# Performance work log

Hardware: AMD Instinct MI355X
Metric: run time of the kernel (lower is better)

## Reference

```python
import jax, jax.numpy as jnp
import numpy as np

D_IN = 1024
D_OUT = 1024
NUM_HEADS = 16
HEAD_DIM = D_OUT // NUM_HEADS


def setup_inputs() -> dict:
    key = jax.random.key(0)
    k_x, k_q, k_k, k_v, k_o = jax.random.split(key, 5)
    # Xavier-uniform-ish init for weights (stored as [d_in, d_out] for x @ W)
    lim = float(np.sqrt(6.0 / (D_IN + D_OUT)) / np.sqrt(2.0))
    lim_o = float(np.sqrt(6.0 / (D_OUT + D_OUT)))
    return {
        "x": jax.random.normal(k_x, (2, 2048, D_IN), dtype=jnp.float32),
        "W_query": jax.random.uniform(k_q, (D_IN, D_OUT), jnp.float32, -lim, lim),
        "W_key": jax.random.uniform(k_k, (D_IN, D_OUT), jnp.float32, -lim, lim),
        "W_value": jax.random.uniform(k_v, (D_IN, D_OUT), jnp.float32, -lim, lim),
        "W_out": jax.random.uniform(k_o, (D_OUT, D_OUT), jnp.float32, -lim_o, lim_o),
        "b_out": jnp.zeros((D_OUT,), dtype=jnp.float32),
    }


def reference(x, W_query, W_key, W_value, W_out, b_out):
    B, S, _ = x.shape
    scale = 1.0 / np.sqrt(HEAD_DIM)

    def split_heads(t):  # [B,S,D] -> [B,H,S,hd]
        return t.reshape(B, S, NUM_HEADS, HEAD_DIM).transpose(0, 2, 1, 3)

    q = split_heads(x @ W_query)
    k = split_heads(x @ W_key)
    v = split_heads(x @ W_value)

    scores = jnp.einsum("bhqd,bhkd->bhqk", q, k) * scale  # [B,H,S,S]
    causal = jnp.tril(jnp.ones((S, S), dtype=bool))  # True = keep
    scores = jnp.where(causal, scores, -jnp.inf)
    weights = jax.nn.softmax(scores, axis=-1)
    ctx = jnp.einsum("bhqk,bhkd->bhqd", weights, v)
    ctx = ctx.transpose(0, 2, 1, 3).reshape(B, S, D_OUT)
    return ctx @ W_out + b_out
```

## Files before the change

kernel.cpp:

```cpp
#include <hip/hip_runtime.h>
#include <hip/hip_bf16.h>


typedef __bf16 bf16_t;
typedef __bf16 bf16x4 __attribute__((ext_vector_type(4)));
typedef __bf16 bf16x8 __attribute__((ext_vector_type(8)));
typedef float f32x4 __attribute__((ext_vector_type(4)));

__device__ __forceinline__ void barrier_lgkm() {
    asm volatile("s_waitcnt lgkmcnt(0)\n\ts_barrier" ::: "memory");
}

__device__ __forceinline__ float exp_pwrite(f32x4 sc[4], bf16_t* Ps,
                                            int wave, int quad, int l16) {
    float part = 0.f;
    int rowbase = (wave * 16 + l16) * 64;
    int gran = (quad & 1) * 4;
    int chi = quad >> 1;
#pragma unroll
    for (int nt = 0; nt < 4; nt++) {
        f32x4 p;
#pragma unroll
        for (int rr = 0; rr < 4; rr++) {
            p[rr] = __builtin_amdgcn_exp2f(sc[nt][rr]);
            part += p[rr];
        }
        bf16x4 pb;
#pragma unroll
        for (int rr = 0; rr < 4; rr++) pb[rr] = (bf16_t)p[rr];
        int cc = (nt * 2 + chi) ^ (l16 & 7);
        *(bf16x4*)(Ps + rowbase + cc * 8 + gran) = pb;
    }
    part += __shfl_xor(part, 16);
    part += __shfl_xor(part, 32);
    return part;
}

__global__ __launch_bounds__(256) void prep_k(
    const float* __restrict__ x, const float* __restrict__ W0,
    const float* __restrict__ W1, const float* __restrict__ W2,
    const float* __restrict__ W3, bf16_t* __restrict__ xb,
    bf16_t* __restrict__ WTs) {
    __shared__ bf16_t T[64][65];
    int t = threadIdx.x;
    int blk = blockIdx.x;
    if (blk < 4096) {
        int i = blk * 256 + t;
        float4 v = ((const float4*)x)[i];
        bf16x4 o;
        o[0] = (bf16_t)v.x; o[1] = (bf16_t)v.y;
        o[2] = (bf16_t)v.z; o[3] = (bf16_t)v.w;
        ((bf16x4*)xb)[i] = o;
        return;
    }
    int jj = blk - 4096;
    int k0 = (jj & 15) * 64, n0 = ((jj >> 4) & 15) * 64, z = jj >> 8;
    const float* W = (z == 0) ? W0 : (z == 1) ? W1 : (z == 2) ? W2 : W3;
    bf16_t* WT = WTs + (size_t)z * 1048576;
#pragma unroll
    for (int c = 0; c < 4; c++) {
        int idx = c * 256 + t;
        int row = idx >> 4, col4 = (idx & 15) * 4;
        float4 v = *(const float4*)(W + (k0 + row) * 1024 + n0 + col4);
        T[row][col4 + 0] = (bf16_t)v.x;
        T[row][col4 + 1] = (bf16_t)v.y;
        T[row][col4 + 2] = (bf16_t)v.z;
        T[row][col4 + 3] = (bf16_t)v.w;
    }
    __syncthreads();
#pragma unroll
    for (int c = 0; c < 4; c++) {
        int idx = c * 256 + t;
        int nrow = idx >> 4, kc4 = (idx & 15) * 4;
        bf16x4 o;
        o[0] = T[kc4 + 0][nrow];
        o[1] = T[kc4 + 1][nrow];
        o[2] = T[kc4 + 2][nrow];
        o[3] = T[kc4 + 3][nrow];
        *(bf16x4*)(WT + (n0 + nrow) * 1024 + k0 + kc4) = o;
    }
}

__global__ __launch_bounds__(256) void qkv_k(
    const bf16_t* __restrict__ xb, const bf16_t* __restrict__ WTs,
    bf16_t* __restrict__ Qb, bf16_t* __restrict__ Kb, bf16_t* __restrict__ Vb) {
    const int KD = 1024;
    __shared__ __align__(16) bf16_t As[2][4096];
    __shared__ __align__(16) bf16_t Bs[2][4096];
    int tid = threadIdx.x;
    int wave = tid >> 6, lane = tid & 63;
    int quad = lane >> 4, l16 = lane & 15;
    int wm = wave >> 1, wn = wave & 1;
    int z = blockIdx.z;
    const bf16_t* BT = WTs + (size_t)z * 1048576;
    int m0 = blockIdx.x * 128;
    int n0 = blockIdx.y * 128;

    int r = tid >> 2;
    int c8 = (((tid & 3) ^ ((tid >> 3) & 3))) * 8;
    const bf16_t* gA0 = xb + (size_t)(m0 + r) * KD + c8;
    const bf16_t* gA1 = xb + (size_t)(m0 + 64 + r) * KD + c8;
    const bf16_t* gB0 = BT + (size_t)(n0 + r) * KD + c8;
    const bf16_t* gB1 = BT + (size_t)(n0 + 64 + r) * KD + c8;

    f32x4 acc[4][4];
#pragma unroll
    for (int i = 0; i < 4; i++)
#pragma unroll
        for (int j = 0; j < 4; j++) acc[i][j] = (f32x4){0.f, 0.f, 0.f, 0.f};

    int4 sa0 = *(const int4*)gA0, sa1 = *(const int4*)gA1;
    int4 sb0 = *(const int4*)gB0, sb1 = *(const int4*)gB1;
    *(int4*)(As[0] + tid * 8) = sa0;
    *(int4*)(As[0] + 2048 + tid * 8) = sa1;
    *(int4*)(Bs[0] + tid * 8) = sb0;
    *(int4*)(Bs[0] + 2048 + tid * 8) = sb1;
    sa0 = *(const int4*)(gA0 + 32); sa1 = *(const int4*)(gA1 + 32);
    sb0 = *(const int4*)(gB0 + 32); sb1 = *(const int4*)(gB1 + 32);

    int csw = (quad ^ ((l16 >> 1) & 3)) * 8;
#pragma unroll 1
    for (int kk = 0; kk < 32; kk += 2) {
        barrier_lgkm();
        bf16x8 af[4], bfr[4];
#pragma unroll
        for (int mt = 0; mt < 4; mt++)
            af[mt] = *(const bf16x8*)(As[0] + (wm * 64 + mt * 16 + l16) * 32 + csw);
#pragma unroll
        for (int nt = 0; nt < 4; nt++)
            bfr[nt] = *(const bf16x8*)(Bs[0] + (wn * 64 + nt * 16 + l16) * 32 + csw);
        *(int4*)(As[1] + tid * 8) = sa0;
        *(int4*)(As[1] + 2048 + tid * 8) = sa1;
        *(int4*)(Bs[1] + tid * 8) = sb0;
        *(int4*)(Bs[1] + 2048 + tid * 8) = sb1;
        if (kk + 2 < 32) {
            int k0 = (kk + 2) * 32;
            sa0 = *(const int4*)(gA0 + k0); sa1 = *(const int4*)(gA1 + k0);
            sb0 = *(const int4*)(gB0 + k0); sb1 = *(const int4*)(gB1 + k0);
        }
        if (z == 2) {
#pragma unroll
            for (int mt = 0; mt < 4; mt++)
#pragma unroll
                for (int nt = 0; nt < 4; nt++)
                    acc[mt][nt] = __builtin_amdgcn_mfma_f32_16x16x32_bf16(
                        bfr[nt], af[mt], acc[mt][nt], 0, 0, 0);
        } else {
#pragma unroll
            for (int mt = 0; mt < 4; mt++)
#pragma unroll
                for (int nt = 0; nt < 4; nt++)
                    acc[mt][nt] = __builtin_amdgcn_mfma_f32_16x16x32_bf16(
                        af[mt], bfr[nt], acc[mt][nt], 0, 0, 0);
        }
        barrier_lgkm();
#pragma unroll
        for (int mt = 0; mt < 4; mt++)
            af[mt] = *(const bf16x8*)(As[1] + (wm * 64 + mt * 16 + l16) * 32 + csw);
#pragma unroll
        for (int nt = 0; nt < 4; nt++)
            bfr[nt] = *(const bf16x8*)(Bs[1] + (wn * 64 + nt * 16 + l16) * 32 + csw);
        if (kk + 2 < 32) {
            *(int4*)(As[0] + tid * 8) = sa0;
            *(int4*)(As[0] + 2048 + tid * 8) = sa1;
            *(int4*)(Bs[0] + tid * 8) = sb0;
            *(int4*)(Bs[0] + 2048 + tid * 8) = sb1;
            if (kk + 3 < 32) {
                int k0 = (kk + 3) * 32;
                sa0 = *(const int4*)(gA0 + k0); sa1 = *(const int4*)(gA1 + k0);
                sb0 = *(const int4*)(gB0 + k0); sb1 = *(const int4*)(gB1 + k0);
            }
        }
        if (z == 2) {
#pragma unroll
            for (int mt = 0; mt < 4; mt++)
#pragma unroll
                for (int nt = 0; nt < 4; nt++)
                    acc[mt][nt] = __builtin_amdgcn_mfma_f32_16x16x32_bf16(
                        bfr[nt], af[mt], acc[mt][nt], 0, 0, 0);
        } else {
#pragma unroll
            for (int mt = 0; mt < 4; mt++)
#pragma unroll
                for (int nt = 0; nt < 4; nt++)
                    acc[mt][nt] = __builtin_amdgcn_mfma_f32_16x16x32_bf16(
                        af[mt], bfr[nt], acc[mt][nt], 0, 0, 0);
        }
    }

    if (z == 0) {
#pragma unroll
        for (int mt = 0; mt < 4; mt++) {
            int mg_base = m0 + wm * 64 + mt * 16 + quad * 4;
#pragma unroll
            for (int nt = 0; nt < 4; nt++) {
                int ng = n0 + wn * 64 + nt * 16 + l16;
                int h = ng >> 6, d = ng & 63;
#pragma unroll
                for (int rr = 0; rr < 4; rr++) {
                    int mg = mg_base + rr;
                    int b = mg >> 11, s = mg & 2047;
                    Qb[(((size_t)(b * 16 + h) * 2048) + s) * 64 + d] =
                        (bf16_t)acc[mt][nt][rr];
                }
            }
        }
    } else if (z == 1) {
#pragma unroll
        for (int mt = 0; mt < 4; mt++) {
            int mg_base = m0 + wm * 64 + mt * 16 + quad * 4;
#pragma unroll
            for (int nt = 0; nt < 4; nt++) {
                int ng = n0 + wn * 64 + nt * 16 + l16;
                int h = ng >> 6, dd = ng & 63;
#pragma unroll
                for (int rr = 0; rr < 4; rr++) {
                    int mg = mg_base + rr;
                    int b = mg >> 11, sl = mg & 2047;
                    int kt = sl >> 6, row = sl & 63;
                    int cc = (dd >> 3) ^ (row & 7);
                    Kb[(size_t)(b * 16 + h) * 131072 + kt * 4096 + row * 64 +
                       cc * 8 + (dd & 7)] = (bf16_t)acc[mt][nt][rr];
                }
            }
        }
    } else {
#pragma unroll
        for (int mt = 0; mt < 4; mt++) {
            int sg = m0 + wm * 64 + mt * 16 + l16;
            int b = sg >> 11, sl = sg & 2047;
            int kt = sl >> 6, srow = sl & 63;
#pragma unroll
            for (int nt = 0; nt < 4; nt++) {
                int dg_base = n0 + wn * 64 + nt * 16 + quad * 4;
#pragma unroll
                for (int rr = 0; rr < 4; rr++) {
                    int dg = dg_base + rr;
                    int h = dg >> 6, dd = dg & 63;
                    int cc = (srow >> 3) ^ (dd & 7);
                    Vb[(size_t)(b * 16 + h) * 131072 + kt * 4096 + dd * 64 +
                       cc * 8 + (srow & 7)] = (bf16_t)acc[mt][nt][rr];
                }
            }
        }
    }
}

__global__ __launch_bounds__(256) void attn_k(
    const bf16_t* __restrict__ Qb, const bf16_t* __restrict__ Kb,
    const bf16_t* __restrict__ Vb, bf16_t* __restrict__ ctxb) {
    const int S = 2048;
    __shared__ __align__(16) bf16_t Ks[2][4096];
    __shared__ __align__(16) bf16_t Vs[2][4096];
    __shared__ __align__(16) bf16_t Ps[2][4096];
    int tid = threadIdx.x, wave = tid >> 6, lane = tid & 63;
    int quad = lane >> 4, l16 = lane & 15;

    int f = blockIdx.x + 32 * blockIdx.y;
    int g = f >> 8, s = f & 255;
    int qtj = g ? (15 - (s & 15)) : (s & 15);
    int bh = (s >> 4) + 16 * g;
    int h = bh & 15, b = bh >> 4;
    int q0 = qtj * 128;

    const bf16_t* Qbh = Qb + (size_t)bh * S * 64;
    const bf16_t* Kbh = Kb + (size_t)bh * 131072;
    const bf16_t* Vbh = Vb + (size_t)bh * 131072;

    const float qs = 0.125f * 1.44269504f;
    bf16x8 aQ[2][2];
#pragma unroll
    for (int sub = 0; sub < 2; sub++) {
        const bf16_t* rq = Qbh + (size_t)(q0 + sub * 64 + wave * 16 + l16) * 64;
#pragma unroll
        for (int ks = 0; ks < 2; ks++) {
            bf16x8 t = *(const bf16x8*)(rq + ks * 32 + quad * 8);
#pragma unroll
            for (int j = 0; j < 8; j++) t[j] = (bf16_t)((float)t[j] * qs);
            aQ[sub][ks] = t;
        }
    }

    float L[2] = {0.f, 0.f};
    f32x4 O[2][4];
#pragma unroll
    for (int sub = 0; sub < 2; sub++)
#pragma unroll
        for (int i = 0; i < 4; i++) O[sub][i] = (f32x4){0.f, 0.f, 0.f, 0.f};

    int tmax = 2 * qtj + 2;
    int4 ska = *(const int4*)(Kbh + tid * 8);
    int4 skb = *(const int4*)(Kbh + 2048 + tid * 8);
    int4 sva = *(const int4*)(Vbh + tid * 8);
    int4 svb = *(const int4*)(Vbh + 2048 + tid * 8);
    *(int4*)(Ks[0] + tid * 8) = ska; *(int4*)(Ks[0] + 2048 + tid * 8) = skb;
    *(int4*)(Vs[0] + tid * 8) = sva; *(int4*)(Vs[0] + 2048 + tid * 8) = svb;
    ska = *(const int4*)(Kbh + 4096 + tid * 8);
    skb = *(const int4*)(Kbh + 6144 + tid * 8);
    sva = *(const int4*)(Vbh + 4096 + tid * 8);
    svb = *(const int4*)(Vbh + 6144 + tid * 8);

#pragma unroll 1
    for (int kt = 0; kt < tmax; kt++) {
        int cur = kt & 1;
        barrier_lgkm();
        bf16x8 kf[4][2], vf[4][2];
#pragma unroll
        for (int nt = 0; nt < 4; nt++) {
            const bf16_t* krow = Ks[cur] + (nt * 16 + l16) * 64;
            const bf16_t* vrow = Vs[cur] + (nt * 16 + l16) * 64;
#pragma unroll
            for (int ks = 0; ks < 2; ks++) {
                int csw = ((ks * 4 + quad) ^ (l16 & 7)) * 8;
                kf[nt][ks] = *(const bf16x8*)(krow + csw);
                vf[nt][ks] = *(const bf16x8*)(vrow + csw);
            }
        }
        if (kt + 1 < tmax) {
            *(int4*)(Ks[cur ^ 1] + tid * 8) = ska;
            *(int4*)(Ks[cur ^ 1] + 2048 + tid * 8) = skb;
            *(int4*)(Vs[cur ^ 1] + tid * 8) = sva;
            *(int4*)(Vs[cur ^ 1] + 2048 + tid * 8) = svb;
        }
        if (kt + 2 < tmax) {
            const bf16_t* kg = Kbh + (kt + 2) * 4096;
            const bf16_t* vg = Vbh + (kt + 2) * 4096;
            ska = *(const int4*)(kg + tid * 8);
            skb = *(const int4*)(kg + 2048 + tid * 8);
            sva = *(const int4*)(vg + tid * 8);
            svb = *(const int4*)(vg + 2048 + tid * 8);
        }

        bool do_lo = (kt < tmax - 1);
        if (do_lo) {
            f32x4 sc[4];
#pragma unroll
            for (int nt = 0; nt < 4; nt++) {
                f32x4 ss = (f32x4){0.f, 0.f, 0.f, 0.f};
                ss = __builtin_amdgcn_mfma_f32_16x16x32_bf16(kf[nt][0], aQ[0][0], ss, 0, 0, 0);
                ss = __builtin_amdgcn_mfma_f32_16x16x32_bf16(kf[nt][1], aQ[0][1], ss, 0, 0, 0);
                sc[nt] = ss;
            }
            if (kt == tmax - 2) {
                int qg = q0 + wave * 16 + l16;
#pragma unroll
                for (int nt = 0; nt < 4; nt++)
#pragma unroll
                    for (int rr = 0; rr < 4; rr++)
                        if (kt * 64 + nt * 16 + quad * 4 + rr > qg) sc[nt][rr] = -1e30f;
            }
            L[0] += exp_pwrite(sc, Ps[0], wave, quad, l16);
        }
        {
            f32x4 sc[4];
#pragma unroll
            for (int nt = 0; nt < 4; nt++) {
                f32x4 ss = (f32x4){0.f, 0.f, 0.f, 0.f};
                ss = __builtin_amdgcn_mfma_f32_16x16x32_bf16(kf[nt][0], aQ[1][0], ss, 0, 0, 0);
                ss = __builtin_amdgcn_mfma_f32_16x16x32_bf16(kf[nt][1], aQ[1][1], ss, 0, 0, 0);
                sc[nt] = ss;
            }
            if (kt == tmax - 1) {
                int qg = q0 + 64 + wave * 16 + l16;
#pragma unroll
                for (int nt = 0; nt < 4; nt++)
#pragma unroll
                    for (int rr = 0; rr < 4; rr++)
                        if (kt * 64 + nt * 16 + quad * 4 + rr > qg) sc[nt][rr] = -1e30f;
            }
            L[1] += exp_pwrite(sc, Ps[1], wave, quad, l16);
        }

#pragma unroll
        for (int ks = 0; ks < 2; ks++) {
            int csw = ((ks * 4 + quad) ^ (l16 & 7)) * 8;
            bf16x8 aPhi = *(const bf16x8*)(Ps[1] + (wave * 16 + l16) * 64 + csw);
            bf16x8 aPlo;
            if (do_lo) aPlo = *(const bf16x8*)(Ps[0] + (wave * 16 + l16) * 64 + csw);
#pragma unroll
            for (int nt = 0; nt < 4; nt++) {
                O[1][nt] = __builtin_amdgcn_mfma_f32_16x16x32_bf16(aPhi, vf[nt][ks],
                                                                   O[1][nt], 0, 0, 0);
                if (do_lo)
                    O[0][nt] = __builtin_amdgcn_mfma_f32_16x16x32_bf16(aPlo, vf[nt][ks],
                                                                       O[0][nt], 0, 0, 0);
            }
        }
    }

#pragma unroll
    for (int sub = 0; sub < 2; sub++) {
        float il[4];
#pragma unroll
        for (int rr = 0; rr < 4; rr++) il[rr] = 1.f / __shfl(L[sub], quad * 4 + rr);
#pragma unroll
        for (int nt = 0; nt < 4; nt++) {
#pragma unroll
            for (int rr = 0; rr < 4; rr++) {
                int qoff = q0 + sub * 64 + wave * 16 + quad * 4 + rr;
                int col = h * 64 + nt * 16 + l16;
                ctxb[(size_t)(b * 2048 + qoff) * 1024 + col] =
                    (bf16_t)(O[sub][nt][rr] * il[rr]);
            }
        }
    }
}

__global__ __launch_bounds__(256) void out_k(
    const bf16_t* __restrict__ ctxb, const bf16_t* __restrict__ WoT,
    const float* __restrict__ bo, float* __restrict__ out) {
    const int KD = 1024;
    __shared__ __align__(16) bf16_t As[2][2048];
    __shared__ __align__(16) bf16_t Bs[2][4096];
    int tid = threadIdx.x;
    int wave = tid >> 6, lane = tid & 63;
    int quad = lane >> 4, l16 = lane & 15;
    int wm = wave >> 1, wn = wave & 1;
    int m0 = blockIdx.x * 64;
    int n0 = blockIdx.y * 128;

    int r = tid >> 2;
    int c8 = (((tid & 3) ^ ((tid >> 3) & 3))) * 8;
    const bf16_t* gA  = ctxb + (size_t)(m0 + r) * KD + c8;
    const bf16_t* gB0 = WoT + (size_t)(n0 + r) * KD + c8;
    const bf16_t* gB1 = WoT + (size_t)(n0 + 64 + r) * KD + c8;

    f32x4 acc[2][4];
#pragma unroll
    for (int i = 0; i < 2; i++)
#pragma unroll
        for (int j = 0; j < 4; j++) acc[i][j] = (f32x4){0.f, 0.f, 0.f, 0.f};

    int4 sa = *(const int4*)gA;
    int4 sb0 = *(const int4*)gB0, sb1 = *(const int4*)gB1;
    *(int4*)(As[0] + tid * 8) = sa;
    *(int4*)(Bs[0] + tid * 8) = sb0;
    *(int4*)(Bs[0] + 2048 + tid * 8) = sb1;
    sa = *(const int4*)(gA + 32);
    sb0 = *(const int4*)(gB0 + 32); sb1 = *(const int4*)(gB1 + 32);

    int csw = (quad ^ ((l16 >> 1) & 3)) * 8;
#pragma unroll 1
    for (int kk = 0; kk < 32; kk += 2) {
        barrier_lgkm();
        bf16x8 af[2], bfr[4];
#pragma unroll
        for (int mt = 0; mt < 2; mt++)
            af[mt] = *(const bf16x8*)(As[0] + (wm * 32 + mt * 16 + l16) * 32 + csw);
#pragma unroll
        for (int nt = 0; nt < 4; nt++)
            bfr[nt] = *(const bf16x8*)(Bs[0] + (wn * 64 + nt * 16 + l16) * 32 + csw);
        *(int4*)(As[1] + tid * 8) = sa;
        *(int4*)(Bs[1] + tid * 8) = sb0;
        *(int4*)(Bs[1] + 2048 + tid * 8) = sb1;
        if (kk + 2 < 32) {
            int k0 = (kk + 2) * 32;
            sa = *(const int4*)(gA + k0);
            sb0 = *(const int4*)(gB0 + k0); sb1 = *(const int4*)(gB1 + k0);
        }
#pragma unroll
        for (int mt = 0; mt < 2; mt++)
#pragma unroll
            for (int nt = 0; nt < 4; nt++)
                acc[mt][nt] = __builtin_amdgcn_mfma_f32_16x16x32_bf16(
                    af[mt], bfr[nt], acc[mt][nt], 0, 0, 0);
        barrier_lgkm();
#pragma unroll
        for (int mt = 0; mt < 2; mt++)
            af[mt] = *(const bf16x8*)(As[1] + (wm * 32 + mt * 16 + l16) * 32 + csw);
#pragma unroll
        for (int nt = 0; nt < 4; nt++)
            bfr[nt] = *(const bf16x8*)(Bs[1] + (wn * 64 + nt * 16 + l16) * 32 + csw);
        if (kk + 2 < 32) {
            *(int4*)(As[0] + tid * 8) = sa;
            *(int4*)(Bs[0] + tid * 8) = sb0;
            *(int4*)(Bs[0] + 2048 + tid * 8) = sb1;
            if (kk + 3 < 32) {
                int k0 = (kk + 3) * 32;
                sa = *(const int4*)(gA + k0);
                sb0 = *(const int4*)(gB0 + k0); sb1 = *(const int4*)(gB1 + k0);
            }
        }
#pragma unroll
        for (int mt = 0; mt < 2; mt++)
#pragma unroll
            for (int nt = 0; nt < 4; nt++)
                acc[mt][nt] = __builtin_amdgcn_mfma_f32_16x16x32_bf16(
                    af[mt], bfr[nt], acc[mt][nt], 0, 0, 0);
    }

#pragma unroll
    for (int mt = 0; mt < 2; mt++) {
        int mg_base = m0 + wm * 32 + mt * 16 + quad * 4;
#pragma unroll
        for (int nt = 0; nt < 4; nt++) {
            int ng = n0 + wn * 64 + nt * 16 + l16;
            float bv = bo[ng];
#pragma unroll
            for (int rr = 0; rr < 4; rr++) {
                int mg = mg_base + rr;
                out[(size_t)mg * 1024 + ng] = acc[mt][nt][rr] + bv;
            }
        }
    }
}

extern "C" void kernel_launch(void* const* d_in, const int* in_sizes, int n_in,
                              void* d_out, int out_size, void* d_ws, size_t ws_size,
                              hipStream_t stream) {
    const float* x  = (const float*)d_in[0];
    const float* Wq = (const float*)d_in[1];
    const float* Wk = (const float*)d_in[2];
    const float* Wv = (const float*)d_in[3];
    const float* Wo = (const float*)d_in[4];
    const float* bo = (const float*)d_in[5];
    float* out = (float*)d_out;
    char* ws = (char*)d_ws;

    bf16_t* xb   = (bf16_t*)ws;
    bf16_t* WTs  = (bf16_t*)(ws + (8u << 20));
    bf16_t* Qb   = (bf16_t*)(ws + (16u << 20));
    bf16_t* Kb   = (bf16_t*)(ws + (24u << 20));
    bf16_t* Vb   = (bf16_t*)(ws + (32u << 20));
    bf16_t* ctxb = (bf16_t*)(ws + (40u << 20));

    prep_k<<<5120, 256, 0, stream>>>(x, Wq, Wk, Wv, Wo, xb, WTs);
    qkv_k<<<dim3(32, 8, 3), 256, 0, stream>>>(xb, WTs, Qb, Kb, Vb);
    attn_k<<<dim3(32, 16), 256, 0, stream>>>(Qb, Kb, Vb, ctxb);
    out_k<<<dim3(64, 8), 256, 0, stream>>>(ctxb, WTs + 3145728, bo, out);
}
```

Measured before the change: 180.4 us.

## Load K/V fragments directly from global memory and remap blocks per XCD

The attention kernel stops staging K and V tiles through double-buffered shared memory with barriers. Each wave now reads its MFMA fragments straight from global memory using precomputed swizzled offsets. The block index mapping is also changed so that blocks sharing the same batch-head land on the same XCD (f&7), which improves L2 reuse of K/V. The change drops LDS traffic and barriers but relies on cache hits and exposes global memory latency inside the loop, since there is no prefetch.

```diff
diff --git a/kernel.cpp b/kernel.cpp
--- a/kernel.cpp
+++ b/kernel.cpp
@@ -250,16 +250,17 @@
     const bf16_t* __restrict__ Qb, const bf16_t* __restrict__ Kb,
     const bf16_t* __restrict__ Vb, bf16_t* __restrict__ ctxb) {
     const int S = 2048;
-    __shared__ __align__(16) bf16_t Ks[2][4096];
-    __shared__ __align__(16) bf16_t Vs[2][4096];
     __shared__ __align__(16) bf16_t Ps[2][4096];
     int tid = threadIdx.x, wave = tid >> 6, lane = tid & 63;
     int quad = lane >> 4, l16 = lane & 15;
 
-    int f = blockIdx.x + 32 * blockIdx.y;
-    int g = f >> 8, s = f & 255;
-    int qtj = g ? (15 - (s & 15)) : (s & 15);
-    int bh = (s >> 4) + 16 * g;
+    int f = blockIdx.x;
+    int xcd = f & 7;
+    int j = f >> 3;
+    int hi = j >> 5;
+    int idx = j & 31;
+    int qtj = hi ? (15 - (idx & 15)) : (idx & 15);
+    int bh = xcd * 4 + ((idx >> 4) + 2 * hi);
     int h = bh & 15, b = bh >> 4;
     int q0 = qtj * 128;
 
@@ -276,7 +277,7 @@
         for (int ks = 0; ks < 2; ks++) {
             bf16x8 t = *(const bf16x8*)(rq + ks * 32 + quad * 8);
 #pragma unroll
-            for (int j = 0; j < 8; j++) t[j] = (bf16_t)((float)t[j] * qs);
+            for (int jj = 0; jj < 8; jj++) t[jj] = (bf16_t)((float)t[jj] * qs);
             aQ[sub][ks] = t;
         }
     }
@@ -288,48 +289,26 @@
 #pragma unroll
         for (int i = 0; i < 4; i++) O[sub][i] = (f32x4){0.f, 0.f, 0.f, 0.f};
 
+    int koff[4][2];
+#pragma unroll
+    for (int nt = 0; nt < 4; nt++)
+#pragma unroll
+        for (int ks = 0; ks < 2; ks++)
+            koff[nt][ks] = (nt * 16 + l16) * 64 + ((ks * 4 + quad) ^ (l16 & 7)) * 8;
+
     int tmax = 2 * qtj + 2;
-    int4 ska = *(const int4*)(Kbh + tid * 8);
-    int4 skb = *(const int4*)(Kbh + 2048 + tid * 8);
-    int4 sva = *(const int4*)(Vbh + tid * 8);
-    int4 svb = *(const int4*)(Vbh + 2048 + tid * 8);
-    *(int4*)(Ks[0] + tid * 8) = ska; *(int4*)(Ks[0] + 2048 + tid * 8) = skb;
-    *(int4*)(Vs[0] + tid * 8) = sva; *(int4*)(Vs[0] + 2048 + tid * 8) = svb;
-    ska = *(const int4*)(Kbh + 4096 + tid * 8);
-    skb = *(const int4*)(Kbh + 6144 + tid * 8);
-    sva = *(const int4*)(Vbh + 4096 + tid * 8);
-    svb = *(const int4*)(Vbh + 6144 + tid * 8);
-
 #pragma unroll 1
     for (int kt = 0; kt < tmax; kt++) {
-        int cur = kt & 1;
-        barrier_lgkm();
+        const bf16_t* kbase = Kbh + kt * 4096;
+        const bf16_t* vbase = Vbh + kt * 4096;
         bf16x8 kf[4][2], vf[4][2];
 #pragma unroll
-        for (int nt = 0; nt < 4; nt++) {
-            const bf16_t* krow = Ks[cur] + (nt * 16 + l16) * 64;
-            const bf16_t* vrow = Vs[cur] + (nt * 16 + l16) * 64;
+        for (int nt = 0; nt < 4; nt++)
 #pragma unroll
             for (int ks = 0; ks < 2; ks++) {
-                int csw = ((ks * 4 + quad) ^ (l16 & 7)) * 8;
-                kf[nt][ks] = *(const bf16x8*)(krow + csw);
-                vf[nt][ks] = *(const bf16x8*)(vrow + csw);
-            }
-        }
-        if (kt + 1 < tmax) {
-            *(int4*)(Ks[cur ^ 1] + tid * 8) = ska;
-            *(int4*)(Ks[cur ^ 1] + 2048 + tid * 8) = skb;
-            *(int4*)(Vs[cur ^ 1] + tid * 8) = sva;
-            *(int4*)(Vs[cur ^ 1] + 2048 + tid * 8) = svb;
-        }
-        if (kt + 2 < tmax) {
-            const bf16_t* kg = Kbh + (kt + 2) * 4096;
-            const bf16_t* vg = Vbh + (kt + 2) * 4096;
-            ska = *(const int4*)(kg + tid * 8);
-            skb = *(const int4*)(kg + 2048 + tid * 8);
-            sva = *(const int4*)(vg + tid * 8);
-            svb = *(const int4*)(vg + 2048 + tid * 8);
-        }
+                kf[nt][ks] = *(const bf16x8*)(kbase + koff[nt][ks]);
+                vf[nt][ks] = *(const bf16x8*)(vbase + koff[nt][ks]);
+            }
 
         bool do_lo = (kt < tmax - 1);
         if (do_lo) {
@@ -526,6 +505,6 @@
 
     prep_k<<<5120, 256, 0, stream>>>(x, Wq, Wk, Wv, Wo, xb, WTs);
     qkv_k<<<dim3(32, 8, 3), 256, 0, stream>>>(xb, WTs, Qb, Kb, Vb);
-    attn_k<<<dim3(32, 16), 256, 0, stream>>>(Qb, Kb, Vb, ctxb);
+    attn_k<<<512, 256, 0, stream>>>(Qb, Kb, Vb, ctxb);
     out_k<<<dim3(64, 8), 256, 0, stream>>>(ctxb, WTs + 3145728, bo, out);
 }
```

Measured after the change: 177.7 us. No clear change (-1.5%).
